# Optimization experiments

Hardware: AMD Instinct MI355X
Metric: run time of the kernel (lower is better)

The kernel has to match this reference:

```python
import jax, jax.numpy as jnp
import numpy as np

DIM = 96
D_STATE = 16
D_CONV = 3
D_INNER = 192   # int(DIM * 2.0)
DT_RANK = 6     # ceil(DIM / 16)
K = 4           # cross-scan directions
BATCH, H, W = 2, 56, 56


def setup_inputs() -> dict:
    key = jax.random.key(0)
    k = jax.random.split(key, 8)
    x = jax.random.normal(k[0], (BATCH, DIM, H, W), jnp.float32)
    W_in = jax.random.normal(k[1], (DIM, 2 * D_INNER), jnp.float32) / np.sqrt(DIM)
    W_conv = jax.random.normal(k[2], (D_INNER, 1, D_CONV, D_CONV), jnp.float32) / D_CONV
    b_conv = jnp.zeros((D_INNER,), jnp.float32)
    W_xproj = jax.random.normal(k[3], (K, D_INNER, DT_RANK + 2 * D_STATE), jnp.float32) / np.sqrt(D_INNER)
    W_dt = jax.random.normal(k[4], (K, DT_RANK, D_INNER), jnp.float32) / np.sqrt(DT_RANK)
    # dt bias init as in torch: dt ~ exp(U * (log 0.1 - log 0.001) + log 0.001), inv-softplus
    dt = jnp.exp(jax.random.uniform(k[5], (K, D_INNER), jnp.float32)
                 * (np.log(0.1) - np.log(0.001)) + np.log(0.001))
    dt = jnp.clip(dt, 1e-4, None)
    b_dt = dt + jnp.log(-jnp.expm1(-dt))
    A_logs = jnp.log(jnp.broadcast_to(jnp.arange(1, D_STATE + 1, dtype=jnp.float32),
                                      (K, D_INNER, D_STATE)))
    Ds = jnp.ones((K, D_INNER), jnp.float32)
    W_out = jax.random.normal(k[6], (D_INNER, DIM), jnp.float32) / np.sqrt(D_INNER)
    return dict(x=x, W_in=W_in, W_conv=W_conv, b_conv=b_conv, W_xproj=W_xproj,
                W_dt=W_dt, b_dt=b_dt, A_logs=A_logs, Ds=Ds, W_out=W_out)


def _ss2d(x, W_in, W_conv, b_conv, W_xproj, W_dt, b_dt, A_logs, Ds, W_out):
    Bsz, C, Hh, Ww = x.shape
    L = Hh * Ww
    # in_proj
    xf = x.transpose(0, 2, 3, 1).reshape(Bsz, L, C)        # (B, L, C)
    xz = xf @ W_in
    xp, z = jnp.split(xz, 2, axis=-1)                       # each (B, L, D)
    # depthwise conv + silu
    xi = xp.reshape(Bsz, Hh, Ww, -1).transpose(0, 3, 1, 2)  # (B, D, H, W)
    pad = D_CONV // 2
    xi = jax.lax.conv_general_dilated(
        xi, W_conv, (1, 1), ((pad, pad), (pad, pad)),
        feature_group_count=xi.shape[1],
        dimension_numbers=('NCHW', 'OIHW', 'NCHW')) + b_conv[None, :, None, None]
    xi = jax.nn.silu(xi)
    D = xi.shape[1]
    # cross-scan: 4 directions, each (B, L, D)
    x1 = xi.reshape(Bsz, D, L).transpose(0, 2, 1)
    x2 = xi[:, :, :, ::-1].reshape(Bsz, D, L).transpose(0, 2, 1)
    xt = xi.transpose(0, 1, 3, 2)                           # (B, D, W, H)
    x3 = xt.reshape(Bsz, D, L).transpose(0, 2, 1)
    x4 = xt[:, :, :, ::-1].reshape(Bsz, D, L).transpose(0, 2, 1)
    xs = jnp.stack([x1, x2, x3, x4])                        # (K, B, L, D)
    # per-direction projections, batched over K
    xdbl = jnp.einsum('kbld,kde->kble', xs, W_xproj)
    dr = xdbl[..., :DT_RANK]
    Bk = xdbl[..., DT_RANK:DT_RANK + D_STATE]               # (K, B, L, N)
    Ck = xdbl[..., DT_RANK + D_STATE:]                      # (K, B, L, N)
    delta = jax.nn.softplus(jnp.einsum('kblr,krd->kbld', dr, W_dt)
                            + b_dt[:, None, None, :])       # (K, B, L, D)
    A = -jnp.exp(A_logs)                                    # (K, D, N)

    def step(h, inp):
        x_i, d_i, B_i, C_i = inp  # (K,B,D), (K,B,D), (K,B,N), (K,B,N)
        dA = jnp.exp(d_i[..., None] * A[:, None])           # (K, B, D, N)
        h = dA * h + (d_i * x_i)[..., None] * B_i[:, :, None, :]
        y = jnp.einsum('kbdn,kbn->kbd', h, C_i)
        return h, y

    h0 = jnp.zeros((K, Bsz, D, D_STATE), xs.dtype)
    seq = (xs.transpose(2, 0, 1, 3), delta.transpose(2, 0, 1, 3),
           Bk.transpose(2, 0, 1, 3), Ck.transpose(2, 0, 1, 3))
    _, ys = jax.lax.scan(step, h0, seq)                     # (L, K, B, D)
    ys = ys.transpose(1, 2, 0, 3) + xs * Ds[:, None, None, :]  # (K, B, L, D)
    # cross-merge back to row-major (h w) order
    y1 = ys[0]
    y2 = ys[1].reshape(Bsz, Hh, Ww, D)[:, :, ::-1, :].reshape(Bsz, L, D)
    y3 = ys[2].reshape(Bsz, Ww, Hh, D).transpose(0, 2, 1, 3).reshape(Bsz, L, D)
    y4 = ys[3].reshape(Bsz, Ww, Hh, D)[:, :, ::-1, :].transpose(0, 2, 1, 3).reshape(Bsz, L, D)
    y = (y1 + y2 + y3 + y4) * jax.nn.silu(z)
    out = (y @ W_out).reshape(Bsz, Hh, Ww, C).transpose(0, 3, 1, 2)
    return out


def reference(x, W_in, W_conv, b_conv, W_xproj, W_dt, b_dt, A_logs, Ds, W_out):
    return _ss2d(x, W_in, W_conv, b_conv, W_xproj, W_dt, b_dt, A_logs, Ds, W_out)
```

## Files before the change

### kernel.cpp

```cpp
#include <hip/hip_runtime.h>
#include <math.h>

constexpr int BATCH  = 2;
constexpr int CDIM   = 96;
constexpr int HH     = 56;
constexpr int WW     = 56;
constexpr int LL     = HH * WW;
constexpr int DIN    = 192;
constexpr int NK     = 4;
constexpr int NST    = 16;
constexpr int RNK    = 6;
constexpr int EPROJ  = RNK + 2 * NST;
constexpr int SCH    = 64;
constexpr int NCH    = LL / SCH;
constexpr int CGRP   = DIN / 16;

constexpr int STDU = SCH + 2;
constexpr int STBC = SCH + 6;
constexpr int STY  = SCH + 4;
constexpr int STB1 = SCH + 4;

constexpr size_t SZ_PX   = (size_t)BATCH * LL * DIN;
constexpr size_t OFF_XP  = 0;
constexpr size_t OFF_Z   = OFF_XP + SZ_PX;
constexpr size_t OFF_XI  = OFF_Z  + SZ_PX;
constexpr size_t OFF_XIT = OFF_XI + SZ_PX;
constexpr size_t OFF_DR  = OFF_XIT + SZ_PX;
constexpr size_t SZ_DR   = (size_t)NK * BATCH * LL * 8;
constexpr size_t OFF_B   = OFF_DR + SZ_DR;
constexpr size_t SZ_BC   = (size_t)NK * BATCH * LL * NST;
constexpr size_t OFF_C   = OFF_B + SZ_BC;
constexpr size_t OFF_YD  = OFF_C + SZ_BC;
constexpr size_t SZ_YD   = (size_t)NK * BATCH * LL * DIN;
constexpr size_t OFF_HE  = OFF_YD + SZ_YD;
constexpr size_t SZ_HS   = (size_t)NK * BATCH * NCH * DIN * NST;
constexpr size_t OFF_HI  = OFF_HE + SZ_HS;
constexpr size_t OFF_WT  = OFF_HI + SZ_HS;

__device__ __forceinline__ float silu(float v) {
    return v / (1.0f + __expf(-v));
}

__device__ __forceinline__ float softplus_f(float x) {
    return (x > 20.0f) ? x : __logf(1.0f + __expf(x));
}

__device__ __forceinline__ int rev56(int l) {
    int r = l % WW;
    return l + 55 - 2 * r;
}

__device__ __forceinline__ float row_reduce16(float p) {
    p += __int_as_float(__builtin_amdgcn_update_dpp(0, __float_as_int(p), 0x128, 0xf, 0xf, true));
    p += __int_as_float(__builtin_amdgcn_update_dpp(0, __float_as_int(p), 0x124, 0xf, 0xf, true));
    p += __int_as_float(__builtin_amdgcn_update_dpp(0, __float_as_int(p), 0x122, 0xf, 0xf, true));
    p += __int_as_float(__builtin_amdgcn_update_dpp(0, __float_as_int(p), 0x121, 0xf, 0xf, true));
    return p;
}

__device__ __forceinline__ size_t hs_idx(int c, int kb, int d, int n) {
    return ((size_t)(c * (NK * BATCH) + kb) * DIN + d) * NST + n;
}

__device__ __forceinline__ float4 delta4(
        float4 r03, float2 r45, const float4* wr, float4 bb4) {
    float4 raw = bb4;
    raw.x = fmaf(r03.x, wr[0].x, raw.x); raw.y = fmaf(r03.x, wr[0].y, raw.y);
    raw.z = fmaf(r03.x, wr[0].z, raw.z); raw.w = fmaf(r03.x, wr[0].w, raw.w);
    raw.x = fmaf(r03.y, wr[1].x, raw.x); raw.y = fmaf(r03.y, wr[1].y, raw.y);
    raw.z = fmaf(r03.y, wr[1].z, raw.z); raw.w = fmaf(r03.y, wr[1].w, raw.w);
    raw.x = fmaf(r03.z, wr[2].x, raw.x); raw.y = fmaf(r03.z, wr[2].y, raw.y);
    raw.z = fmaf(r03.z, wr[2].z, raw.z); raw.w = fmaf(r03.z, wr[2].w, raw.w);
    raw.x = fmaf(r03.w, wr[3].x, raw.x); raw.y = fmaf(r03.w, wr[3].y, raw.y);
    raw.z = fmaf(r03.w, wr[3].z, raw.z); raw.w = fmaf(r03.w, wr[3].w, raw.w);
    raw.x = fmaf(r45.x, wr[4].x, raw.x); raw.y = fmaf(r45.x, wr[4].y, raw.y);
    raw.z = fmaf(r45.x, wr[4].z, raw.z); raw.w = fmaf(r45.x, wr[4].w, raw.w);
    raw.x = fmaf(r45.y, wr[5].x, raw.x); raw.y = fmaf(r45.y, wr[5].y, raw.y);
    raw.z = fmaf(r45.y, wr[5].z, raw.z); raw.w = fmaf(r45.y, wr[5].w, raw.w);
    raw.x = softplus_f(raw.x); raw.y = softplus_f(raw.y);
    raw.z = softplus_f(raw.z); raw.w = softplus_f(raw.w);
    return raw;
}

constexpr int K1_PIX = 8;
__global__ __launch_bounds__(384) void k_inproj(
        const float* __restrict__ x, const float* __restrict__ W_in,
        const float* __restrict__ W_xproj,
        float* __restrict__ xp, float* __restrict__ z, float* __restrict__ Wt) {
    __shared__ float sxT[CDIM][K1_PIX];
    int gp0 = blockIdx.x * K1_PIX;
    int t   = threadIdx.x;
    int b   = gp0 / LL;
    int l0  = gp0 - b * LL;
    int gid = blockIdx.x * 384 + t;
    if (gid < NK * DIN * EPROJ) {
        int k = gid / (DIN * EPROJ);
        int r = gid % (DIN * EPROJ);
        int d = r / EPROJ;
        int e = r % EPROJ;
        Wt[((size_t)k * EPROJ + e) * DIN + d] = W_xproj[gid];
    }
    for (int i = t; i < CDIM * K1_PIX; i += 384) {
        int c = i >> 3, p = i & 7;
        sxT[c][p] = x[((size_t)(b * CDIM + c)) * LL + l0 + p];
    }
    __syncthreads();
    int e = t;
    float acc[K1_PIX];
#pragma unroll
    for (int p = 0; p < K1_PIX; p++) acc[p] = 0.0f;
    const float4* sx4 = (const float4*)sxT;
#pragma unroll 4
    for (int c = 0; c < CDIM; c++) {
        float w  = W_in[c * (2 * DIN) + e];
        float4 va = sx4[2 * c];
        float4 vb = sx4[2 * c + 1];
        acc[0] = fmaf(va.x, w, acc[0]); acc[1] = fmaf(va.y, w, acc[1]);
        acc[2] = fmaf(va.z, w, acc[2]); acc[3] = fmaf(va.w, w, acc[3]);
        acc[4] = fmaf(vb.x, w, acc[4]); acc[5] = fmaf(vb.y, w, acc[5]);
        acc[6] = fmaf(vb.z, w, acc[6]); acc[7] = fmaf(vb.w, w, acc[7]);
    }
    if (e < DIN) {
#pragma unroll
        for (int p = 0; p < K1_PIX; p++)
            xp[((size_t)(gp0 + p)) * DIN + e] = acc[p];
    } else {
        int e2 = e - DIN;
#pragma unroll
        for (int p = 0; p < K1_PIX; p++)
            z[((size_t)(gp0 + p)) * DIN + e2] = acc[p];
    }
}

__global__ __launch_bounds__(192) void k_conv(
        const float* __restrict__ xp, const float* __restrict__ Wc,
        const float* __restrict__ bc, float* __restrict__ xi,
        float* __restrict__ xiT) {
    int gp = blockIdx.x;
    int d  = threadIdx.x;
    int b  = gp / LL;
    int l  = gp - b * LL;
    int h  = l / WW;
    int w  = l - h * WW;
    float acc = bc[d];
#pragma unroll
    for (int dy = -1; dy <= 1; dy++) {
        int hh = h + dy;
        if (hh < 0 || hh >= HH) continue;
#pragma unroll
        for (int dx = -1; dx <= 1; dx++) {
            int ww = w + dx;
            if (ww < 0 || ww >= WW) continue;
            acc = fmaf(xp[((size_t)b * LL + hh * WW + ww) * DIN + d],
                       Wc[d * 9 + (dy + 1) * 3 + (dx + 1)], acc);
        }
    }
    float v = silu(acc);
    xi [(size_t)gp * DIN + d] = v;
    int m = w * HH + h;
    xiT[((size_t)b * LL + m) * DIN + d] = v;
}

constexpr int K3_PIX = 32;
__global__ __launch_bounds__(256) void k_xproj(
        const float* __restrict__ xi, const float* __restrict__ xiT,
        const float* __restrict__ Wt,
        float* __restrict__ drbuf, float* __restrict__ Bbuf,
        float* __restrict__ Cbuf) {
    __shared__ float4 v4[K3_PIX][49];
    __shared__ float4 sw4[EPROJ][49];
    int k   = blockIdx.y;
    int gp0 = blockIdx.x * K3_PIX;
    int b   = gp0 / LL;
    int l0  = gp0 - b * LL;
    int t   = threadIdx.x;
    const float* src = (k >= 2) ? xiT : xi;
    const float4* xin4 = (const float4*)(src + (size_t)gp0 * DIN);
    for (int i = t; i < K3_PIX * 48; i += 256)
        v4[i / 48][i % 48] = xin4[i];
    const float4* wt4 = (const float4*)(Wt + (size_t)k * EPROJ * DIN);
    for (int i = t; i < EPROJ * 48; i += 256)
        sw4[i / 48][i % 48] = wt4[i];
    __syncthreads();
    int p0 = t & 15;
    int eg = t >> 4;
    bool has3 = (eg < EPROJ - 32);
    float acc[2][3] = {{0.f, 0.f, 0.f}, {0.f, 0.f, 0.f}};
    for (int j = 0; j < 48; j++) {
        float4 w0 = sw4[eg][j];
        float4 w1 = sw4[eg + 16][j];
        float4 w2 = has3 ? sw4[eg + 32][j] : make_float4(0.f, 0.f, 0.f, 0.f);
#pragma unroll
        for (int q = 0; q < 2; q++) {
            float4 vv = v4[p0 + 16 * q][j];
            acc[q][0] = fmaf(vv.x, w0.x, acc[q][0]); acc[q][0] = fmaf(vv.y, w0.y, acc[q][0]);
            acc[q][0] = fmaf(vv.z, w0.z, acc[q][0]); acc[q][0] = fmaf(vv.w, w0.w, acc[q][0]);
            acc[q][1] = fmaf(vv.x, w1.x, acc[q][1]); acc[q][1] = fmaf(vv.y, w1.y, acc[q][1]);
            acc[q][1] = fmaf(vv.z, w1.z, acc[q][1]); acc[q][1] = fmaf(vv.w, w1.w, acc[q][1]);
            acc[q][2] = fmaf(vv.x, w2.x, acc[q][2]); acc[q][2] = fmaf(vv.y, w2.y, acc[q][2]);
            acc[q][2] = fmaf(vv.z, w2.z, acc[q][2]); acc[q][2] = fmaf(vv.w, w2.w, acc[q][2]);
        }
    }
#pragma unroll
    for (int q = 0; q < 2; q++) {
        int m  = l0 + p0 + 16 * q;
        int ls = (k & 1) ? rev56(m) : m;
        size_t kb  = (size_t)(k * BATCH + b);
        size_t b8  = (kb * LL + ls) * 8;
        size_t b16 = (kb * LL + ls) * NST;
        if (eg < RNK) drbuf[b8 + eg] = acc[q][0];
        else          Bbuf[b16 + eg - RNK] = acc[q][0];
        int e1 = eg + 16;
        if (e1 < RNK + NST) Bbuf[b16 + e1 - RNK] = acc[q][1];
        else                Cbuf[b16 + e1 - RNK - NST] = acc[q][1];
        if (has3) Cbuf[b16 + eg + 32 - RNK - NST] = acc[q][2];
    }
}

__global__ __launch_bounds__(256) void k_scanA(
        const float* __restrict__ xi, const float* __restrict__ xiT,
        const float* __restrict__ drbuf,
        const float* __restrict__ Bbuf, const float* __restrict__ A_logs,
        const float* __restrict__ W_dt, const float* __restrict__ b_dt,
        float* __restrict__ Pbuf, float* __restrict__ hend) {
    __shared__ float2 sDU2[16][STDU];
    __shared__ float  sB1t[16][STB1];
    int c   = blockIdx.x;
    int blk = blockIdx.y;
    int k   = blk / (BATCH * CGRP);
    int rem = blk % (BATCH * CGRP);
    int b   = rem / CGRP;
    int cg  = rem % CGRP;
    int d0  = cg * 16;
    int t    = threadIdx.x;
    int lane = t & 63, wave = t >> 6;
    int grp  = lane >> 4, n = lane & 15;
    int ch   = wave * 4 + grp;
    int d    = d0 + ch;
    float A = -__expf(A_logs[((size_t)(k * DIN + d)) * NST + n]);
    size_t kb = (size_t)(k * BATCH + b);
    const float* drp = drbuf + kb * LL * 8;
    const float* bp  = Bbuf  + kb * LL * NST;
    const float* ub  = ((k >= 2) ? xiT : xi) + (size_t)b * LL * DIN;
    int ss  = t >> 2;
    int cc0 = (t & 3) * 4;
    float4 wr[RNK];
#pragma unroll
    for (int r = 0; r < RNK; r++)
        wr[r] = *(const float4*)(W_dt + ((size_t)k * RNK + r) * DIN + d0 + cc0);
    float4 bb4 = *(const float4*)(b_dt + k * DIN + d0 + cc0);
    int l0 = c * SCH;
    {
        int l    = l0 + ss;
        int ridx = (k & 1) ? rev56(l) : l;
        float4 r03 = *(const float4*)(drp + (size_t)l * 8);
        float2 r45 = *(const float2*)(drp + (size_t)l * 8 + 4);
        float4 dlt = delta4(r03, r45, wr, bb4);
        float4 u4  = *(const float4*)(ub + (size_t)ridx * DIN + d0 + cc0);
        float4 B4  = *(const float4*)(bp + (size_t)l * NST + cc0);
        sDU2[cc0 + 0][ss] = make_float2(dlt.x, dlt.x * u4.x);
        sDU2[cc0 + 1][ss] = make_float2(dlt.y, dlt.y * u4.y);
        sDU2[cc0 + 2][ss] = make_float2(dlt.z, dlt.z * u4.z);
        sDU2[cc0 + 3][ss] = make_float2(dlt.w, dlt.w * u4.w);
        sB1t[cc0 + 0][ss] = B4.x;
        sB1t[cc0 + 1][ss] = B4.y;
        sB1t[cc0 + 2][ss] = B4.z;
        sB1t[cc0 + 3][ss] = B4.w;
    }
    __syncthreads();
    float h = 0.0f, P = 1.0f;
#pragma unroll 2
    for (int s4 = 0; s4 < SCH; s4 += 4) {
        float4 duA = *(const float4*)&sDU2[ch][s4];
        float4 duB = *(const float4*)&sDU2[ch][s4 + 2];
        float4 bq  = *(const float4*)&sB1t[n][s4];
        float dA;
        dA = __expf(duA.x * A); h = fmaf(dA, h, duA.y * bq.x); P *= dA;
        dA = __expf(duA.z * A); h = fmaf(dA, h, duA.w * bq.y); P *= dA;
        dA = __expf(duB.x * A); h = fmaf(dA, h, duB.y * bq.z); P *= dA;
        dA = __expf(duB.z * A); h = fmaf(dA, h, duB.w * bq.w); P *= dA;
    }
    size_t idx = hs_idx(c, (int)kb, d, n);
    Pbuf[idx] = P;
    hend[idx] = h;
}

__global__ __launch_bounds__(256) void k_scanB(
        const float* __restrict__ Pbuf, const float* __restrict__ hend,
        float* __restrict__ hin) {
    int tid = blockIdx.x * 256 + threadIdx.x;
    int kb  = tid / (DIN * NST);
    int dn  = tid % (DIN * NST);
    float h = 0.0f;
    for (int c = 0; c < NCH; c++) {
        size_t idx = ((size_t)(c * (NK * BATCH) + kb)) * (DIN * NST) + dn;
        hin[idx] = h;
        h = fmaf(Pbuf[idx], h, hend[idx]);
    }
}

__global__ __launch_bounds__(256) void k_scanC(
        const float* __restrict__ xi, const float* __restrict__ xiT,
        const float* __restrict__ drbuf,
        const float* __restrict__ Bbuf, const float* __restrict__ Cbuf,
        const float* __restrict__ A_logs, const float* __restrict__ W_dt,
        const float* __restrict__ b_dt, const float* __restrict__ hin,
        float* __restrict__ ydir) {
    __shared__ float2 sDU2[16][STDU];
    __shared__ float2 sBC2[16][STBC];
    __shared__ float  sY[16][STY];
    int c   = blockIdx.x;
    int blk = blockIdx.y;
    int k   = blk / (BATCH * CGRP);
    int rem = blk % (BATCH * CGRP);
    int b   = rem / CGRP;
    int cg  = rem % CGRP;
    int d0  = cg * 16;
    int t    = threadIdx.x;
    int lane = t & 63, wave = t >> 6;
    int grp  = lane >> 4, n = lane & 15;
    int ch   = wave * 4 + grp;
    int d    = d0 + ch;
    float A = -__expf(A_logs[((size_t)(k * DIN + d)) * NST + n]);
    size_t kb = (size_t)(k * BATCH + b);
    const float* drp = drbuf + kb * LL * 8;
    const float* bp  = Bbuf  + kb * LL * NST;
    const float* cp  = Cbuf  + kb * LL * NST;
    const float* ub  = ((k >= 2) ? xiT : xi) + (size_t)b * LL * DIN;
    float*       yp  = ydir  + kb * LL * DIN;
    int ss  = t >> 2;
    int cc0 = (t & 3) * 4;
    float4 wr[RNK];
#pragma unroll
    for (int r = 0; r < RNK; r++)
        wr[r] = *(const float4*)(W_dt + ((size_t)k * RNK + r) * DIN + d0 + cc0);
    float4 bb4 = *(const float4*)(b_dt + k * DIN + d0 + cc0);
    int l0 = c * SCH;
    {
        int l    = l0 + ss;
        int ridx = (k & 1) ? rev56(l) : l;
        float4 r03 = *(const float4*)(drp + (size_t)l * 8);
        float2 r45 = *(const float2*)(drp + (size_t)l * 8 + 4);
        float4 dlt = delta4(r03, r45, wr, bb4);
        float4 u4  = *(const float4*)(ub + (size_t)ridx * DIN + d0 + cc0);
        float4 B4  = *(const float4*)(bp + (size_t)l * NST + cc0);
        float4 C4  = *(const float4*)(cp + (size_t)l * NST + cc0);
        sDU2[cc0 + 0][ss] = make_float2(dlt.x, dlt.x * u4.x);
        sDU2[cc0 + 1][ss] = make_float2(dlt.y, dlt.y * u4.y);
        sDU2[cc0 + 2][ss] = make_float2(dlt.z, dlt.z * u4.z);
        sDU2[cc0 + 3][ss] = make_float2(dlt.w, dlt.w * u4.w);
        sBC2[cc0 + 0][ss] = make_float2(B4.x, C4.x);
        sBC2[cc0 + 1][ss] = make_float2(B4.y, C4.y);
        sBC2[cc0 + 2][ss] = make_float2(B4.z, C4.z);
        sBC2[cc0 + 3][ss] = make_float2(B4.w, C4.w);
    }
    float h = hin[hs_idx(c, (int)kb, d, n)];
    __syncthreads();
#pragma unroll 2
    for (int s4 = 0; s4 < SCH; s4 += 4) {
        float4 duA = *(const float4*)&sDU2[ch][s4];
        float4 duB = *(const float4*)&sDU2[ch][s4 + 2];
        float4 bcA = *(const float4*)&sBC2[n][s4];
        float4 bcB = *(const float4*)&sBC2[n][s4 + 2];
        float dA, y0, y1, y2, y3;
        dA = __expf(duA.x * A); h = fmaf(dA, h, duA.y * bcA.x); y0 = row_reduce16(h * bcA.y);
        dA = __expf(duA.z * A); h = fmaf(dA, h, duA.w * bcA.z); y1 = row_reduce16(h * bcA.w);
        dA = __expf(duB.x * A); h = fmaf(dA, h, duB.y * bcB.x); y2 = row_reduce16(h * bcB.y);
        dA = __expf(duB.z * A); h = fmaf(dA, h, duB.w * bcB.z); y3 = row_reduce16(h * bcB.w);
        if (n == 0) *(float4*)&sY[ch][s4] = make_float4(y0, y1, y2, y3);
    }
    __syncthreads();
    for (int i = t; i < SCH * 16; i += 256) {
        int s = i >> 4, cc = i & 15;
        int l = l0 + s;
        int sidx = (k & 1) ? rev56(l) : l;
        yp[(size_t)sidx * DIN + d0 + cc] = sY[cc][s];
    }
}

constexpr int K5_PIX = 8;
__global__ __launch_bounds__(192) void k_out(
        const float* __restrict__ ydir, const float* __restrict__ xi,
        const float* __restrict__ zbuf, const float* __restrict__ Ds,
        const float* __restrict__ W_out, float* __restrict__ out) {
    __shared__ float g[DIN][12];
    __shared__ float so[CDIM][9];
    int gp0 = blockIdx.x * K5_PIX;
    int b   = gp0 / LL;
    int l0  = gp0 - b * LL;
    int t   = threadIdx.x;
    for (int i = t; i < K5_PIX * DIN; i += 192) {
        int p = i / DIN, dd = i % DIN;
        int l = l0 + p;
        int h = l / WW, w = l - h * WW;
        int m = w * HH + h;
        size_t offL = ((size_t)b * LL + l) * DIN + dd;
        size_t offM = ((size_t)b * LL + m) * DIN + dd;
        float y = ydir[offL] + ydir[SZ_PX + offL]
                + ydir[2 * SZ_PX + offM] + ydir[3 * SZ_PX + offM];
        float dsum = Ds[dd] + Ds[DIN + dd] + Ds[2 * DIN + dd] + Ds[3 * DIN + dd];
        y = fmaf(xi[offL], dsum, y);
        g[dd][p] = y * silu(zbuf[offL]);
    }
    __syncthreads();
    int f    = t % CDIM;
    int half = t / CDIM;
    float acc[4] = {0.f, 0.f, 0.f, 0.f};
#pragma unroll 4
    for (int dd = 0; dd < DIN; dd++) {
        float wv = W_out[dd * CDIM + f];
        float4 gv = *(const float4*)&g[dd][half * 4];
        acc[0] = fmaf(gv.x, wv, acc[0]);
        acc[1] = fmaf(gv.y, wv, acc[1]);
        acc[2] = fmaf(gv.z, wv, acc[2]);
        acc[3] = fmaf(gv.w, wv, acc[3]);
    }
#pragma unroll
    for (int p = 0; p < 4; p++) so[f][half * 4 + p] = acc[p];
    __syncthreads();
    for (int i = t; i < CDIM * K5_PIX; i += 192) {
        int f2 = i / K5_PIX, p2 = i % K5_PIX;
        out[((size_t)(b * CDIM + f2)) * LL + l0 + p2] = so[f2][p2];
    }
}

extern "C" void kernel_launch(void* const* d_in, const int* in_sizes, int n_in,
                              void* d_out, int out_size, void* d_ws, size_t ws_size,
                              hipStream_t stream) {
    const float* x       = (const float*)d_in[0];
    const float* W_in    = (const float*)d_in[1];
    const float* W_conv  = (const float*)d_in[2];
    const float* b_conv  = (const float*)d_in[3];
    const float* W_xproj = (const float*)d_in[4];
    const float* W_dt    = (const float*)d_in[5];
    const float* b_dt    = (const float*)d_in[6];
    const float* A_logs  = (const float*)d_in[7];
    const float* Ds      = (const float*)d_in[8];
    const float* W_out   = (const float*)d_in[9];
    float* out = (float*)d_out;
    float* ws  = (float*)d_ws;

    float* xp    = ws + OFF_XP;
    float* z     = ws + OFF_Z;
    float* xi    = ws + OFF_XI;
    float* xiT   = ws + OFF_XIT;
    float* drbuf = ws + OFF_DR;
    float* Bbuf  = ws + OFF_B;
    float* Cbuf  = ws + OFF_C;
    float* ydir  = ws + OFF_YD;
    float* hend  = ws + OFF_HE;
    float* hin   = ws + OFF_HI;
    float* Wt    = ws + OFF_WT;
    float* Pbuf  = xp;

    k_inproj<<<(BATCH * LL) / K1_PIX, 384, 0, stream>>>(x, W_in, W_xproj, xp, z, Wt);
    k_conv<<<BATCH * LL, DIN, 0, stream>>>(xp, W_conv, b_conv, xi, xiT);
    dim3 g3((BATCH * LL) / K3_PIX, NK);
    k_xproj<<<g3, 256, 0, stream>>>(xi, xiT, Wt, drbuf, Bbuf, Cbuf);
    dim3 gs(NCH, NK * BATCH * CGRP);
    k_scanA<<<gs, 256, 0, stream>>>(xi, xiT, drbuf, Bbuf, A_logs, W_dt, b_dt, Pbuf, hend);
    k_scanB<<<(NK * BATCH * DIN * NST) / 256, 256, 0, stream>>>(Pbuf, hend, hin);
    k_scanC<<<gs, 256, 0, stream>>>(xi, xiT, drbuf, Bbuf, Cbuf, A_logs, W_dt, b_dt, hin, ydir);
    k_out<<<(BATCH * LL) / K5_PIX, 192, 0, stream>>>(ydir, xi, z, Ds, W_out, out);
}
```

Before: 210.7 us.

## Remap scanC threads to two states per lane with 32-channel blocks

The chunk-output scan kernel now maps 8 lanes per channel, each holding two state elements, so reductions need only three DPP steps instead of four. Each block covers 32 channels instead of 16 and processes its 64-step chunk in two 32-step halves to keep shared memory small. This halves the block count and amortizes B/C loads across more channels, at the cost of more serial work per thread and extra barriers.

```diff
diff --git a/kernel.cpp b/kernel.cpp
--- a/kernel.cpp
+++ b/kernel.cpp
@@ -15,9 +15,14 @@
 constexpr int NCH    = LL / SCH;
 constexpr int CGRP   = DIN / 16;
 
+constexpr int CG2  = 32;
+constexpr int NCG2 = DIN / CG2;
+constexpr int HCH  = 32;
+constexpr int SDU2 = HCH + 2;
+constexpr int SBC2 = HCH + 2;
+constexpr int SY2  = HCH + 4;
+
 constexpr int STDU = SCH + 2;
-constexpr int STBC = SCH + 6;
-constexpr int STY  = SCH + 4;
 constexpr int STB1 = SCH + 4;
 
 constexpr size_t SZ_PX   = (size_t)BATCH * LL * DIN;
@@ -50,11 +55,24 @@
     return l + 55 - 2 * r;
 }
 
+template <int CTRL>
+__device__ __forceinline__ float dpp_add(float p) {
+    return p + __int_as_float(__builtin_amdgcn_update_dpp(
+        0, __float_as_int(p), CTRL, 0xf, 0xf, true));
+}
+
 __device__ __forceinline__ float row_reduce16(float p) {
-    p += __int_as_float(__builtin_amdgcn_update_dpp(0, __float_as_int(p), 0x128, 0xf, 0xf, true));
-    p += __int_as_float(__builtin_amdgcn_update_dpp(0, __float_as_int(p), 0x124, 0xf, 0xf, true));
-    p += __int_as_float(__builtin_amdgcn_update_dpp(0, __float_as_int(p), 0x122, 0xf, 0xf, true));
-    p += __int_as_float(__builtin_amdgcn_update_dpp(0, __float_as_int(p), 0x121, 0xf, 0xf, true));
+    p = dpp_add<0x128>(p);
+    p = dpp_add<0x124>(p);
+    p = dpp_add<0x122>(p);
+    p = dpp_add<0x121>(p);
+    return p;
+}
+
+__device__ __forceinline__ float row_reduce8(float p) {
+    p = dpp_add<0xB1>(p);
+    p = dpp_add<0x4E>(p);
+    p = dpp_add<0x141>(p);
     return p;
 }
 
@@ -306,75 +324,98 @@
         const float* __restrict__ A_logs, const float* __restrict__ W_dt,
         const float* __restrict__ b_dt, const float* __restrict__ hin,
         float* __restrict__ ydir) {
-    __shared__ float2 sDU2[16][STDU];
-    __shared__ float2 sBC2[16][STBC];
-    __shared__ float  sY[16][STY];
+    __shared__ float2 sDU[CG2][SDU2];
+    __shared__ float2 sBC[NST][SBC2];
+    __shared__ float  sY[CG2][SY2];
     int c   = blockIdx.x;
     int blk = blockIdx.y;
-    int k   = blk / (BATCH * CGRP);
-    int rem = blk % (BATCH * CGRP);
-    int b   = rem / CGRP;
-    int cg  = rem % CGRP;
-    int d0  = cg * 16;
+    int k   = blk / (BATCH * NCG2);
+    int rem = blk % (BATCH * NCG2);
+    int b   = rem / NCG2;
+    int cg  = rem % NCG2;
+    int d0  = cg * CG2;
     int t    = threadIdx.x;
-    int lane = t & 63, wave = t >> 6;
-    int grp  = lane >> 4, n = lane & 15;
-    int ch   = wave * 4 + grp;
+    int lane = t & 63, w = t >> 6;
+    int g    = lane & 7;
+    int chL  = lane >> 3;
+    int ch   = w * 8 + chL;
     int d    = d0 + ch;
-    float A = -__expf(A_logs[((size_t)(k * DIN + d)) * NST + n]);
-    size_t kb = (size_t)(k * BATCH + b);
+    size_t kb  = (size_t)(k * BATCH + b);
+    size_t adL = ((size_t)(k * DIN + d)) * NST;
+    float A_a = -__expf(A_logs[adL + g]);
+    float A_b = -__expf(A_logs[adL + g + 8]);
     const float* drp = drbuf + kb * LL * 8;
     const float* bp  = Bbuf  + kb * LL * NST;
     const float* cp  = Cbuf  + kb * LL * NST;
     const float* ub  = ((k >= 2) ? xiT : xi) + (size_t)b * LL * DIN;
     float*       yp  = ydir  + kb * LL * DIN;
-    int ss  = t >> 2;
-    int cc0 = (t & 3) * 4;
+    float h_a = hin[hs_idx(c, (int)kb, d, g)];
+    float h_b = hin[hs_idx(c, (int)kb, d, g + 8)];
+    int ss  = t >> 3;
+    int c40 = (t & 7) * 4;
+    int sb  = t >> 2;
+    int n40 = (t & 3) * 4;
     float4 wr[RNK];
 #pragma unroll
     for (int r = 0; r < RNK; r++)
-        wr[r] = *(const float4*)(W_dt + ((size_t)k * RNK + r) * DIN + d0 + cc0);
-    float4 bb4 = *(const float4*)(b_dt + k * DIN + d0 + cc0);
-    int l0 = c * SCH;
-    {
-        int l    = l0 + ss;
-        int ridx = (k & 1) ? rev56(l) : l;
-        float4 r03 = *(const float4*)(drp + (size_t)l * 8);
-        float2 r45 = *(const float2*)(drp + (size_t)l * 8 + 4);
-        float4 dlt = delta4(r03, r45, wr, bb4);
-        float4 u4  = *(const float4*)(ub + (size_t)ridx * DIN + d0 + cc0);
-        float4 B4  = *(const float4*)(bp + (size_t)l * NST + cc0);
-        float4 C4  = *(const float4*)(cp + (size_t)l * NST + cc0);
-        sDU2[cc0 + 0][ss] = make_float2(dlt.x, dlt.x * u4.x);
-        sDU2[cc0 + 1][ss] = make_float2(dlt.y, dlt.y * u4.y);
-        sDU2[cc0 + 2][ss] = make_float2(dlt.z, dlt.z * u4.z);
-        sDU2[cc0 + 3][ss] = make_float2(dlt.w, dlt.w * u4.w);
-        sBC2[cc0 + 0][ss] = make_float2(B4.x, C4.x);
-        sBC2[cc0 + 1][ss] = make_float2(B4.y, C4.y);
-        sBC2[cc0 + 2][ss] = make_float2(B4.z, C4.z);
-        sBC2[cc0 + 3][ss] = make_float2(B4.w, C4.w);
-    }
-    float h = hin[hs_idx(c, (int)kb, d, n)];
-    __syncthreads();
+        wr[r] = *(const float4*)(W_dt + ((size_t)k * RNK + r) * DIN + d0 + c40);
+    float4 bb4 = *(const float4*)(b_dt + k * DIN + d0 + c40);
+
+    for (int half = 0; half < 2; half++) {
+        int l0h = c * SCH + half * HCH;
+        {
+            int l    = l0h + ss;
+            int ridx = (k & 1) ? rev56(l) : l;
+            float4 r03 = *(const float4*)(drp + (size_t)l * 8);
+            float2 r45 = *(const float2*)(drp + (size_t)l * 8 + 4);
+            float4 dlt = delta4(r03, r45, wr, bb4);
+            float4 u4  = *(const float4*)(ub + (size_t)ridx * DIN + d0 + c40);
+            sDU[c40 + 0][ss] = make_float2(dlt.x, dlt.x * u4.x);
+            sDU[c40 + 1][ss] = make_float2(dlt.y, dlt.y * u4.y);
+            sDU[c40 + 2][ss] = make_float2(dlt.z, dlt.z * u4.z);
+            sDU[c40 + 3][ss] = make_float2(dlt.w, dlt.w * u4.w);
+        }
+        if (t < 128) {
+            int l = l0h + sb;
+            float4 B4 = *(const float4*)(bp + (size_t)l * NST + n40);
+            float4 C4 = *(const float4*)(cp + (size_t)l * NST + n40);
+            sBC[n40 + 0][sb] = make_float2(B4.x, C4.x);
+            sBC[n40 + 1][sb] = make_float2(B4.y, C4.y);
+            sBC[n40 + 2][sb] = make_float2(B4.z, C4.z);
+            sBC[n40 + 3][sb] = make_float2(B4.w, C4.w);
+        }
+        __syncthreads();
 #pragma unroll 2
-    for (int s4 = 0; s4 < SCH; s4 += 4) {
-        float4 duA = *(const float4*)&sDU2[ch][s4];
-        float4 duB = *(const float4*)&sDU2[ch][s4 + 2];
-        float4 bcA = *(const float4*)&sBC2[n][s4];
-        float4 bcB = *(const float4*)&sBC2[n][s4 + 2];
-        float dA, y0, y1, y2, y3;
-        dA = __expf(duA.x * A); h = fmaf(dA, h, duA.y * bcA.x); y0 = row_reduce16(h * bcA.y);
-        dA = __expf(duA.z * A); h = fmaf(dA, h, duA.w * bcA.z); y1 = row_reduce16(h * bcA.w);
-        dA = __expf(duB.x * A); h = fmaf(dA, h, duB.y * bcB.x); y2 = row_reduce16(h * bcB.y);
-        dA = __expf(duB.z * A); h = fmaf(dA, h, duB.w * bcB.z); y3 = row_reduce16(h * bcB.w);
-        if (n == 0) *(float4*)&sY[ch][s4] = make_float4(y0, y1, y2, y3);
-    }
-    __syncthreads();
-    for (int i = t; i < SCH * 16; i += 256) {
-        int s = i >> 4, cc = i & 15;
-        int l = l0 + s;
-        int sidx = (k & 1) ? rev56(l) : l;
-        yp[(size_t)sidx * DIN + d0 + cc] = sY[cc][s];
+        for (int s4 = 0; s4 < HCH; s4 += 4) {
+            float4 duA = *(const float4*)&sDU[ch][s4];
+            float4 duB = *(const float4*)&sDU[ch][s4 + 2];
+            float4 aAa = *(const float4*)&sBC[g][s4];
+            float4 aBa = *(const float4*)&sBC[g][s4 + 2];
+            float4 aAb = *(const float4*)&sBC[g + 8][s4];
+            float4 aBb = *(const float4*)&sBC[g + 8][s4 + 2];
+            float dA, p, y0, y1, y2, y3;
+            dA = __expf(duA.x * A_a); h_a = fmaf(dA, h_a, duA.y * aAa.x);
+            dA = __expf(duA.x * A_b); h_b = fmaf(dA, h_b, duA.y * aAb.x);
+            p = h_a * aAa.y; p = fmaf(h_b, aAb.y, p); y0 = row_reduce8(p);
+            dA = __expf(duA.z * A_a); h_a = fmaf(dA, h_a, duA.w * aAa.z);
+            dA = __expf(duA.z * A_b); h_b = fmaf(dA, h_b, duA.w * aAb.z);
+            p = h_a * aAa.w; p = fmaf(h_b, aAb.w, p); y1 = row_reduce8(p);
+            dA = __expf(duB.x * A_a); h_a = fmaf(dA, h_a, duB.y * aBa.x);
+            dA = __expf(duB.x * A_b); h_b = fmaf(dA, h_b, duB.y * aBb.x);
+            p = h_a * aBa.y; p = fmaf(h_b, aBb.y, p); y2 = row_reduce8(p);
+            dA = __expf(duB.z * A_a); h_a = fmaf(dA, h_a, duB.w * aBa.z);
+            dA = __expf(duB.z * A_b); h_b = fmaf(dA, h_b, duB.w * aBb.z);
+            p = h_a * aBa.w; p = fmaf(h_b, aBb.w, p); y3 = row_reduce8(p);
+            if (g == 0) *(float4*)&sY[ch][s4] = make_float4(y0, y1, y2, y3);
+        }
+        __syncthreads();
+        for (int i = t; i < CG2 * HCH; i += 256) {
+            int s = i >> 5, cc = i & 31;
+            int l = l0h + s;
+            int sidx = (k & 1) ? rev56(l) : l;
+            yp[(size_t)sidx * DIN + d0 + cc] = sY[cc][s];
+        }
+        __syncthreads();
     }
 }
 
@@ -460,6 +501,7 @@
     dim3 gs(NCH, NK * BATCH * CGRP);
     k_scanA<<<gs, 256, 0, stream>>>(xi, xiT, drbuf, Bbuf, A_logs, W_dt, b_dt, Pbuf, hend);
     k_scanB<<<(NK * BATCH * DIN * NST) / 256, 256, 0, stream>>>(Pbuf, hend, hin);
-    k_scanC<<<gs, 256, 0, stream>>>(xi, xiT, drbuf, Bbuf, Cbuf, A_logs, W_dt, b_dt, hin, ydir);
+    dim3 gs2(NCH, NK * BATCH * NCG2);
+    k_scanC<<<gs2, 256, 0, stream>>>(xi, xiT, drbuf, Bbuf, Cbuf, A_logs, W_dt, b_dt, hin, ydir);
     k_out<<<(BATCH * LL) / K5_PIX, 192, 0, stream>>>(ydir, xi, z, Ds, W_out, out);
 }
```

Measured after the change: 207.9 us. About the same (-1.4%).
